# Performance work log

Measured on AMD Instinct MI355X. Metric: run time of the kernel, lower is better.

Reference implementation:

```python
import jax, jax.numpy as jnp
import numpy as np

N, D_MODEL, D_HIDDEN = 2048, 4096, 32768

def setup_inputs() -> dict:
    key = jax.random.key(0)
    k1, k2, k3, k4 = jax.random.split(key, 4)
    x = jax.random.normal(k1, (N, D_MODEL), dtype=jnp.float32)
    W_enc = jax.random.normal(k2, (D_MODEL, D_HIDDEN), dtype=jnp.float32) * 0.02
    b_enc = jax.random.normal(k3, (D_HIDDEN,), dtype=jnp.float32) * 0.02
    b_dec = jax.random.normal(k4, (D_MODEL,), dtype=jnp.float32) * 0.02
    return {"x": x, "W_enc": W_enc, "b_enc": b_enc, "b_dec": b_dec, "k": 64}

def reference(x, W_enc, b_enc, b_dec, k):
    # pre-activation: (x - b_dec) @ W_enc + b_enc   -> [N, d_hidden]
    pre_act = (x - b_dec) @ W_enc + b_enc
    acts = jax.nn.relu(pre_act)
    vals, idx = jax.lax.top_k(acts, k)          # [N, k] each
    rows = jnp.arange(acts.shape[0])[:, None]    # [N, 1]
    sparse_features = jnp.zeros_like(pre_act).at[rows, idx].set(vals)
    return sparse_features
```

## Files before the change

kernel.cpp:

```cpp
#include <hip/hip_runtime.h>
#include <hip/hip_fp16.h>

#define DEV __device__ __forceinline__

typedef __attribute__((ext_vector_type(8))) _Float16 half8;
typedef __attribute__((ext_vector_type(4))) _Float16 half4;
typedef __attribute__((ext_vector_type(4))) float floatx4;

static constexpr int M = 2048;
static constexpr int N = 32768;
static constexpr int K = 4096;

DEV void async_copy16(void* lds, const void* g) {
  __builtin_amdgcn_global_load_lds(
      (const __attribute__((address_space(1))) unsigned int*)g,
      (__attribute__((address_space(3))) unsigned int*)lds, 16, 0, 0);
}

__global__ void prep_x(const float* __restrict__ x, const float* __restrict__ b_dec,
                       _Float16* __restrict__ A1, _Float16* __restrict__ A2) {
  int i = blockIdx.x * blockDim.x + threadIdx.x;
  int idx = i * 4;
  float4 xv = *(const float4*)(x + idx);
  float4 bd = *(const float4*)(b_dec + (idx & (K - 1)));
  float c[4] = {xv.x - bd.x, xv.y - bd.y, xv.z - bd.z, xv.w - bd.w};
  half4 a1, a2;
#pragma unroll
  for (int j = 0; j < 4; ++j) {
    float s = c[j] * 0.03125f;
    _Float16 h1 = (_Float16)s;
    a1[j] = h1;
    a2[j] = (_Float16)((s - (float)h1) * 4096.0f);
  }
  *(half4*)(A1 + idx) = a1;
  *(half4*)(A2 + idx) = a2;
}

__global__ void prep_w(const float* __restrict__ W, _Float16* __restrict__ W1T,
                       _Float16* __restrict__ W2T) {
  __shared__ float tile[64][68];
  int tid = threadIdx.x;
  int tn = blockIdx.x & 511, tk = blockIdx.x >> 9;
  int k0 = tk * 64, n0 = tn * 64;
#pragma unroll
  for (int p = 0; p < 4; ++p) {
    int row = p * 16 + (tid >> 4);
    int col = (tid & 15) * 4;
    float4 v = *(const float4*)(W + (size_t)(k0 + row) * N + n0 + col);
    tile[row][col] = v.x; tile[row][col + 1] = v.y;
    tile[row][col + 2] = v.z; tile[row][col + 3] = v.w;
  }
  __syncthreads();
  int nl = tid >> 2, kc = (tid & 3) * 16;
  half8 v1[2], v2[2];
#pragma unroll
  for (int j = 0; j < 16; ++j) {
    float w = tile[kc + j][nl] * 32.0f;
    _Float16 h1 = (_Float16)w;
    _Float16 h2 = (_Float16)((w - (float)h1) * 4096.0f);
    v1[j >> 3][j & 7] = h1;
    v2[j >> 3][j & 7] = h2;
  }
  size_t off = (size_t)(n0 + nl) * K + k0 + kc;
  *(half8*)(W1T + off) = v1[0];
  *(half8*)(W1T + off + 8) = v1[1];
  *(half8*)(W2T + off) = v2[0];
  *(half8*)(W2T + off + 8) = v2[1];
}

__global__ __launch_bounds__(256) void gemm1(
    const _Float16* __restrict__ A, const _Float16* __restrict__ B,
    const float* __restrict__ b_enc, float* __restrict__ out) {
  __shared__ __align__(16) _Float16 lA[128 * 64];
  __shared__ __align__(16) _Float16 lB[128 * 64];
  const int tid = threadIdx.x;
  const int lane = tid & 63, wave = tid >> 6;
  const int wm = wave & 1, wn = wave >> 1;
  const int m0 = (blockIdx.x & 15) * 128, n0 = (blockIdx.x >> 4) * 128;

  floatx4 acc[4][4];
#pragma unroll
  for (int a = 0; a < 4; ++a)
#pragma unroll
    for (int b = 0; b < 4; ++b) acc[a][b] = (floatx4){0.f, 0.f, 0.f, 0.f};

  const int srow = lane >> 3;
  const int spos = lane & 7;
  const int quad = lane >> 4, l16 = lane & 15;

  for (int kk = 0; kk < K; kk += 64) {
#pragma unroll
    for (int i = 0; i < 4; ++i) {
      int ci = wave * 4 + i;
      int r = ci * 8 + srow;
      int ca = spos ^ srow;
      async_copy16(&lA[ci * 512], A + (size_t)(m0 + r) * K + kk + ca * 8);
      async_copy16(&lB[ci * 512], B + (size_t)(n0 + r) * K + kk + ca * 8);
    }
    __syncthreads();
#pragma unroll
    for (int s = 0; s < 2; ++s) {
      half8 af[4], bf[4];
#pragma unroll
      for (int f = 0; f < 4; ++f) {
        int row = wm * 64 + f * 16 + l16;
        int ch = ((s << 2) + quad) ^ (row & 7);
        af[f] = *(const half8*)&lA[row * 64 + ch * 8];
      }
#pragma unroll
      for (int f = 0; f < 4; ++f) {
        int row = wn * 64 + f * 16 + l16;
        int ch = ((s << 2) + quad) ^ (row & 7);
        bf[f] = *(const half8*)&lB[row * 64 + ch * 8];
      }
#pragma unroll
      for (int fm = 0; fm < 4; ++fm)
#pragma unroll
        for (int fn = 0; fn < 4; ++fn)
          acc[fm][fn] = __builtin_amdgcn_mfma_f32_16x16x32_f16(
              af[fm], bf[fn], acc[fm][fn], 0, 0, 0);
    }
    __syncthreads();
  }
  float bv[4];
#pragma unroll
  for (int fn = 0; fn < 4; ++fn) bv[fn] = b_enc[n0 + wn * 64 + fn * 16 + l16];
#pragma unroll
  for (int fm = 0; fm < 4; ++fm) {
    int rbase = m0 + wm * 64 + fm * 16 + quad * 4;
#pragma unroll
    for (int i = 0; i < 4; ++i) {
      float* orow = out + (size_t)(rbase + i) * N + n0 + wn * 64 + l16;
#pragma unroll
      for (int fn = 0; fn < 4; ++fn) orow[fn * 16] = acc[fm][fn][i] + bv[fn];
    }
  }
}

__global__ __launch_bounds__(256) void select_refine(
    const _Float16* __restrict__ A1, const _Float16* __restrict__ A2,
    const _Float16* __restrict__ W1T, const _Float16* __restrict__ W2T,
    const float* __restrict__ b_enc, float* __restrict__ out) {
  __shared__ int hist[4096];
  __shared__ __align__(16) _Float16 a1r[4096];
  __shared__ __align__(16) _Float16 a2r[4096];
  __shared__ float cval[256];
  __shared__ int cidx[256];
  __shared__ int gsum[256];
  __shared__ int Tbin, cnt;

  const int tid = threadIdx.x;
  const int row = blockIdx.x;
  float* rp = out + (size_t)row * N;

  const half8* a1g = (const half8*)(A1 + (size_t)row * K);
  const half8* a2g = (const half8*)(A2 + (size_t)row * K);
  for (int j = tid; j < K / 8; j += 256) {
    ((half8*)a1r)[j] = a1g[j];
    ((half8*)a2r)[j] = a2g[j];
  }
  for (int j = tid; j < 4096; j += 256) hist[j] = 0;
  if (tid == 0) { Tbin = 1; cnt = 0; }
  __syncthreads();

  for (int j = tid; j < N; j += 256) {
    float v = rp[j];
    if (v > 0.f) atomicAdd(&hist[__float_as_uint(v) >> 19], 1);
  }
  __syncthreads();
  int own = 0;
#pragma unroll
  for (int j = 0; j < 16; ++j) own += hist[tid * 16 + j];
  gsum[tid] = own;
  __syncthreads();
  for (int off = 1; off < 256; off <<= 1) {
    int add = (tid + off < 256) ? gsum[tid + off] : 0;
    __syncthreads();
    gsum[tid] += add;
    __syncthreads();
  }
  int acc = gsum[tid] - own;
  for (int j = 15; j >= 0; --j) {
    int h = hist[tid * 16 + j];
    acc += h;
    if (acc >= 64 && acc - h < 64) Tbin = tid * 16 + j;
  }
  __syncthreads();
  float thr = __uint_as_float((unsigned)Tbin << 19) - 0.01f;
  for (int j = tid; j < N; j += 256) {
    float v = rp[j];
    if (v > 0.f && v >= thr) {
      int p = atomicAdd(&cnt, 1);
      if (p < 256) cidx[p] = j;
    }
  }
  __syncthreads();
  const int nc = cnt < 256 ? cnt : 256;

  const int wave = tid >> 6, lane = tid & 63;
  for (int c = wave; c < nc; c += 4) {
    const int col = cidx[c];
    const half8* w1 = (const half8*)(W1T + (size_t)col * K);
    const half8* w2 = (const half8*)(W2T + (size_t)col * K);
    float a = 0.f;
#pragma unroll
    for (int j = 0; j < 8; ++j) {
      int off = j * 64 + lane;
      half8 hw1 = w1[off], hw2 = w2[off];
      half8 ha1 = ((const half8*)a1r)[off], ha2 = ((const half8*)a2r)[off];
#pragma unroll
      for (int e = 0; e < 8; ++e) {
        float sx = fmaf((float)ha2[e], 2.44140625e-4f, (float)ha1[e]);
        float tw = fmaf((float)hw2[e], 2.44140625e-4f, (float)hw1[e]);
        a = fmaf(sx, tw, a);
      }
    }
#pragma unroll
    for (int off = 32; off >= 1; off >>= 1) a += __shfl_xor(a, off);
    if (lane == 0) cval[c] = a + b_enc[col];
  }
  __syncthreads();

  float4 z = {0.f, 0.f, 0.f, 0.f};
  float4* rp4 = (float4*)rp;
  for (int j = tid; j < N / 4; j += 256) rp4[j] = z;
  __syncthreads();
  if (tid < nc) {
    float vi = cval[tid];
    int ii = cidx[tid];
    int rank = 0;
    for (int j = 0; j < nc; ++j) {
      float vj = cval[j];
      rank += (vj > vi) || (vj == vi && cidx[j] < ii);
    }
    if (rank < 64) rp[ii] = vi;
  }
}

extern "C" void kernel_launch(void* const* d_in, const int* in_sizes, int n_in,
                              void* d_out, int out_size, void* d_ws, size_t ws_size,
                              hipStream_t stream) {
  const float* x = (const float*)d_in[0];
  const float* W = (const float*)d_in[1];
  const float* b_enc = (const float*)d_in[2];
  const float* b_dec = (const float*)d_in[3];
  float* out = (float*)d_out;

  _Float16* A1 = (_Float16*)d_ws;
  _Float16* A2 = A1 + (size_t)M * K;
  _Float16* W1T = A2 + (size_t)M * K;
  _Float16* W2T = W1T + (size_t)N * K;

  prep_x<<<(M * K / 4) / 256, 256, 0, stream>>>(x, b_dec, A1, A2);
  prep_w<<<(N / 64) * (K / 64), 256, 0, stream>>>(W, W1T, W2T);
  gemm1<<<(M / 128) * (N / 128), 256, 0, stream>>>(A1, W1T, b_enc, out);
  select_refine<<<M, 256, 0, stream>>>(A1, A2, W1T, W2T, b_enc, out);
}
```

Before: 2.289 ms.

## Rewrite fp16 GEMM with 256x256 tiles, double-buffered async LDS pipeline

Result: faster. 2.205 ms (-3.7%).

```diff
diff --git a/kernel.cpp b/kernel.cpp
--- a/kernel.cpp
+++ b/kernel.cpp
@@ -68,66 +68,157 @@
   *(half8*)(W2T + off + 8) = v2[1];
 }
 
-__global__ __launch_bounds__(256) void gemm1(
+__global__ __launch_bounds__(512, 2) void gemm1(
     const _Float16* __restrict__ A, const _Float16* __restrict__ B,
     const float* __restrict__ b_enc, float* __restrict__ out) {
-  __shared__ __align__(16) _Float16 lA[128 * 64];
-  __shared__ __align__(16) _Float16 lB[128 * 64];
+  __shared__ __align__(16) _Float16 sA[2][256 * 32];
+  __shared__ __align__(16) _Float16 sB[2][256 * 32];
+
   const int tid = threadIdx.x;
   const int lane = tid & 63, wave = tid >> 6;
-  const int wm = wave & 1, wn = wave >> 1;
-  const int m0 = (blockIdx.x & 15) * 128, n0 = (blockIdx.x >> 4) * 128;
-
-  floatx4 acc[4][4];
-#pragma unroll
-  for (int a = 0; a < 4; ++a)
+  const int wm = wave >> 2, wn = wave & 3;
+  const int l16 = lane & 15, quad = lane >> 4;
+
+  const int swz = (blockIdx.x & 7) * 128 + (blockIdx.x >> 3);
+  const int m0 = (swz & 7) * 256, n0 = (swz >> 3) * 256;
+
+  floatx4 acc[8][4];
+#pragma unroll
+  for (int a = 0; a < 8; ++a)
 #pragma unroll
     for (int b = 0; b < 4; ++b) acc[a][b] = (floatx4){0.f, 0.f, 0.f, 0.f};
 
-  const int srow = lane >> 3;
-  const int spos = lane & 7;
-  const int quad = lane >> 4, l16 = lane & 15;
-
-  for (int kk = 0; kk < K; kk += 64) {
-#pragma unroll
-    for (int i = 0; i < 4; ++i) {
-      int ci = wave * 4 + i;
-      int r = ci * 8 + srow;
-      int ca = spos ^ srow;
-      async_copy16(&lA[ci * 512], A + (size_t)(m0 + r) * K + kk + ca * 8);
-      async_copy16(&lB[ci * 512], B + (size_t)(n0 + r) * K + kk + ca * 8);
-    }
-    __syncthreads();
-#pragma unroll
-    for (int s = 0; s < 2; ++s) {
-      half8 af[4], bf[4];
-#pragma unroll
-      for (int f = 0; f < 4; ++f) {
-        int row = wm * 64 + f * 16 + l16;
-        int ch = ((s << 2) + quad) ^ (row & 7);
-        af[f] = *(const half8*)&lA[row * 64 + ch * 8];
-      }
-#pragma unroll
-      for (int f = 0; f < 4; ++f) {
-        int row = wn * 64 + f * 16 + l16;
-        int ch = ((s << 2) + quad) ^ (row & 7);
-        bf[f] = *(const half8*)&lB[row * 64 + ch * 8];
-      }
-#pragma unroll
-      for (int fm = 0; fm < 4; ++fm)
-#pragma unroll
-        for (int fn = 0; fn < 4; ++fn)
-          acc[fm][fn] = __builtin_amdgcn_mfma_f32_16x16x32_f16(
-              af[fm], bf[fn], acc[fm][fn], 0, 0, 0);
-    }
-    __syncthreads();
-  }
+  const int srow = lane >> 2;
+  const int schunk = (lane & 3) ^ ((lane >> 3) & 3);
+  const int rg0 = (wave * 2 + 0) * 16 + srow;
+  const int rg1 = (wave * 2 + 1) * 16 + srow;
+  const _Float16* gA0 = A + (size_t)(m0 + rg0) * K + schunk * 8;
+  const _Float16* gA1 = A + (size_t)(m0 + rg1) * K + schunk * 8;
+  const _Float16* gB0 = B + (size_t)(n0 + rg0) * K + schunk * 8;
+  const _Float16* gB1 = B + (size_t)(n0 + rg1) * K + schunk * 8;
+  const int dG0 = (wave * 2 + 0) * 16 * 32;
+  const int dG1 = (wave * 2 + 1) * 16 * 32;
+
+  const int rslot = (quad ^ ((l16 >> 1) & 3)) * 8;
+  const int aoff = (wm * 128 + l16) * 32 + rslot;
+  const int boff = (wn * 64 + l16) * 32 + rslot;
+
+  async_copy16(&sA[0][dG0], gA0);
+  async_copy16(&sA[0][dG1], gA1);
+  async_copy16(&sB[0][dG0], gB0);
+  async_copy16(&sB[0][dG1], gB1);
+  async_copy16(&sB[1][dG0], gB0 + 32);
+  async_copy16(&sB[1][dG1], gB1 + 32);
+  asm volatile("s_waitcnt vmcnt(2)" ::: "memory");
+  __builtin_amdgcn_s_barrier();
+
+  constexpr int NS = K / 32;
+  half8 af[4], bf[4];
+
+  for (int s = 0; s < NS - 2; ++s) {
+    const int cur = s & 1;
+#pragma unroll
+    for (int f = 0; f < 4; ++f)
+      af[f] = *(const half8*)(sA[cur] + aoff + f * 512);
+#pragma unroll
+    for (int f = 0; f < 4; ++f)
+      bf[f] = *(const half8*)(sB[cur] + boff + f * 512);
+    async_copy16(&sA[cur ^ 1][dG0], gA0 + (s + 1) * 32);
+    async_copy16(&sA[cur ^ 1][dG1], gA1 + (s + 1) * 32);
+    __builtin_amdgcn_s_setprio(1);
+#pragma unroll
+    for (int fm = 0; fm < 4; ++fm)
+#pragma unroll
+      for (int fn = 0; fn < 4; ++fn)
+        acc[fm][fn] = __builtin_amdgcn_mfma_f32_16x16x32_f16(
+            af[fm], bf[fn], acc[fm][fn], 0, 0, 0);
+    __builtin_amdgcn_s_setprio(0);
+    asm volatile("s_waitcnt lgkmcnt(0)" ::: "memory");
+    __builtin_amdgcn_s_barrier();
+#pragma unroll
+    for (int f = 0; f < 4; ++f)
+      af[f] = *(const half8*)(sA[cur] + aoff + 2048 + f * 512);
+    async_copy16(&sB[cur][dG0], gB0 + (s + 2) * 32);
+    async_copy16(&sB[cur][dG1], gB1 + (s + 2) * 32);
+    __builtin_amdgcn_s_setprio(1);
+#pragma unroll
+    for (int fm = 0; fm < 4; ++fm)
+#pragma unroll
+      for (int fn = 0; fn < 4; ++fn)
+        acc[4 + fm][fn] = __builtin_amdgcn_mfma_f32_16x16x32_f16(
+            af[fm], bf[fn], acc[4 + fm][fn], 0, 0, 0);
+    __builtin_amdgcn_s_setprio(0);
+    asm volatile("s_waitcnt vmcnt(2) lgkmcnt(0)" ::: "memory");
+    __builtin_amdgcn_s_barrier();
+  }
+
+  {
+    const int cur = (NS - 2) & 1;
+#pragma unroll
+    for (int f = 0; f < 4; ++f)
+      af[f] = *(const half8*)(sA[cur] + aoff + f * 512);
+#pragma unroll
+    for (int f = 0; f < 4; ++f)
+      bf[f] = *(const half8*)(sB[cur] + boff + f * 512);
+    async_copy16(&sA[cur ^ 1][dG0], gA0 + (NS - 1) * 32);
+    async_copy16(&sA[cur ^ 1][dG1], gA1 + (NS - 1) * 32);
+    __builtin_amdgcn_s_setprio(1);
+#pragma unroll
+    for (int fm = 0; fm < 4; ++fm)
+#pragma unroll
+      for (int fn = 0; fn < 4; ++fn)
+        acc[fm][fn] = __builtin_amdgcn_mfma_f32_16x16x32_f16(
+            af[fm], bf[fn], acc[fm][fn], 0, 0, 0);
+    __builtin_amdgcn_s_setprio(0);
+    asm volatile("s_waitcnt lgkmcnt(0)" ::: "memory");
+    __builtin_amdgcn_s_barrier();
+#pragma unroll
+    for (int f = 0; f < 4; ++f)
+      af[f] = *(const half8*)(sA[cur] + aoff + 2048 + f * 512);
+    __builtin_amdgcn_s_setprio(1);
+#pragma unroll
+    for (int fm = 0; fm < 4; ++fm)
+#pragma unroll
+      for (int fn = 0; fn < 4; ++fn)
+        acc[4 + fm][fn] = __builtin_amdgcn_mfma_f32_16x16x32_f16(
+            af[fm], bf[fn], acc[4 + fm][fn], 0, 0, 0);
+    __builtin_amdgcn_s_setprio(0);
+    asm volatile("s_waitcnt vmcnt(0) lgkmcnt(0)" ::: "memory");
+    __builtin_amdgcn_s_barrier();
+  }
+  {
+    const int cur = (NS - 1) & 1;
+#pragma unroll
+    for (int f = 0; f < 4; ++f)
+      af[f] = *(const half8*)(sA[cur] + aoff + f * 512);
+#pragma unroll
+    for (int f = 0; f < 4; ++f)
+      bf[f] = *(const half8*)(sB[cur] + boff + f * 512);
+    __builtin_amdgcn_s_setprio(1);
+#pragma unroll
+    for (int fm = 0; fm < 4; ++fm)
+#pragma unroll
+      for (int fn = 0; fn < 4; ++fn)
+        acc[fm][fn] = __builtin_amdgcn_mfma_f32_16x16x32_f16(
+            af[fm], bf[fn], acc[fm][fn], 0, 0, 0);
+#pragma unroll
+    for (int f = 0; f < 4; ++f)
+      af[f] = *(const half8*)(sA[cur] + aoff + 2048 + f * 512);
+#pragma unroll
+    for (int fm = 0; fm < 4; ++fm)
+#pragma unroll
+      for (int fn = 0; fn < 4; ++fn)
+        acc[4 + fm][fn] = __builtin_amdgcn_mfma_f32_16x16x32_f16(
+            af[fm], bf[fn], acc[4 + fm][fn], 0, 0, 0);
+    __builtin_amdgcn_s_setprio(0);
+  }
+
   float bv[4];
 #pragma unroll
   for (int fn = 0; fn < 4; ++fn) bv[fn] = b_enc[n0 + wn * 64 + fn * 16 + l16];
 #pragma unroll
-  for (int fm = 0; fm < 4; ++fm) {
-    int rbase = m0 + wm * 64 + fm * 16 + quad * 4;
+  for (int fm = 0; fm < 8; ++fm) {
+    const int rbase = m0 + wm * 128 + fm * 16 + quad * 4;
 #pragma unroll
     for (int i = 0; i < 4; ++i) {
       float* orow = out + (size_t)(rbase + i) * N + n0 + wn * 64 + l16;
@@ -253,6 +344,6 @@
 
   prep_x<<<(M * K / 4) / 256, 256, 0, stream>>>(x, b_dec, A1, A2);
   prep_w<<<(N / 64) * (K / 64), 256, 0, stream>>>(W, W1T, W2T);
-  gemm1<<<(M / 128) * (N / 128), 256, 0, stream>>>(A1, W1T, b_enc, out);
+  gemm1<<<(M / 256) * (N / 256), 512, 0, stream>>>(A1, W1T, b_enc, out);
   select_refine<<<M, 256, 0, stream>>>(A1, A2, W1T, W2T, b_enc, out);
 }
```

## Rewrite gemm1 as 256x256-tile, 4-stage async-LDS pipelined kernel with 8 waves

Applied to the files above, without the earlier changes.

Measured after the change: 2.047 ms. 1.12x faster.

```diff
diff --git a/kernel.cpp b/kernel.cpp
--- a/kernel.cpp
+++ b/kernel.cpp
@@ -16,6 +16,12 @@
       (const __attribute__((address_space(1))) unsigned int*)g,
       (__attribute__((address_space(3))) unsigned int*)lds, 16, 0, 0);
 }
+
+#define BAR() __builtin_amdgcn_s_barrier()
+#define LGKM0() asm volatile("s_waitcnt lgkmcnt(0)" ::: "memory")
+#define VMW(n) asm volatile("s_waitcnt vmcnt(" #n ")" ::: "memory")
+#define PRIO1() __builtin_amdgcn_s_setprio(1)
+#define PRIO0() __builtin_amdgcn_s_setprio(0)
 
 __global__ void prep_x(const float* __restrict__ x, const float* __restrict__ b_dec,
                        _Float16* __restrict__ A1, _Float16* __restrict__ A2) {
@@ -68,66 +74,127 @@
   *(half8*)(W2T + off + 8) = v2[1];
 }
 
-__global__ __launch_bounds__(256) void gemm1(
+__global__ __launch_bounds__(512, 2) void gemm1(
     const _Float16* __restrict__ A, const _Float16* __restrict__ B,
     const float* __restrict__ b_enc, float* __restrict__ out) {
-  __shared__ __align__(16) _Float16 lA[128 * 64];
-  __shared__ __align__(16) _Float16 lB[128 * 64];
+  __shared__ __align__(16) _Float16 sA[4][8192];
+  __shared__ __align__(16) _Float16 sB[4][8192];
+
   const int tid = threadIdx.x;
   const int lane = tid & 63, wave = tid >> 6;
-  const int wm = wave & 1, wn = wave >> 1;
-  const int m0 = (blockIdx.x & 15) * 128, n0 = (blockIdx.x >> 4) * 128;
-
-  floatx4 acc[4][4];
-#pragma unroll
-  for (int a = 0; a < 4; ++a)
+  const int wm = wave >> 2, wn = wave & 3;
+  const int l16 = lane & 15, quad = lane >> 4;
+
+  const int swz = (blockIdx.x & 7) * 128 + (blockIdx.x >> 3);
+  const int m0 = (swz & 7) * 256, n0 = (swz >> 3) * 256;
+
+  floatx4 acc[8][4];
+#pragma unroll
+  for (int a = 0; a < 8; ++a)
 #pragma unroll
     for (int b = 0; b < 4; ++b) acc[a][b] = (floatx4){0.f, 0.f, 0.f, 0.f};
 
-  const int srow = lane >> 3;
-  const int spos = lane & 7;
-  const int quad = lane >> 4, l16 = lane & 15;
-
-  for (int kk = 0; kk < K; kk += 64) {
-#pragma unroll
-    for (int i = 0; i < 4; ++i) {
-      int ci = wave * 4 + i;
-      int r = ci * 8 + srow;
-      int ca = spos ^ srow;
-      async_copy16(&lA[ci * 512], A + (size_t)(m0 + r) * K + kk + ca * 8);
-      async_copy16(&lB[ci * 512], B + (size_t)(n0 + r) * K + kk + ca * 8);
-    }
-    __syncthreads();
-#pragma unroll
-    for (int s = 0; s < 2; ++s) {
-      half8 af[4], bf[4];
-#pragma unroll
-      for (int f = 0; f < 4; ++f) {
-        int row = wm * 64 + f * 16 + l16;
-        int ch = ((s << 2) + quad) ^ (row & 7);
-        af[f] = *(const half8*)&lA[row * 64 + ch * 8];
-      }
-#pragma unroll
-      for (int f = 0; f < 4; ++f) {
-        int row = wn * 64 + f * 16 + l16;
-        int ch = ((s << 2) + quad) ^ (row & 7);
-        bf[f] = *(const half8*)&lB[row * 64 + ch * 8];
-      }
-#pragma unroll
-      for (int fm = 0; fm < 4; ++fm)
-#pragma unroll
-        for (int fn = 0; fn < 4; ++fn)
-          acc[fm][fn] = __builtin_amdgcn_mfma_f32_16x16x32_f16(
-              af[fm], bf[fn], acc[fm][fn], 0, 0, 0);
-    }
-    __syncthreads();
-  }
+  const int srow = lane >> 2;
+  const int schunk = (lane & 3) ^ ((lane >> 3) & 3);
+  const _Float16* pA = A + (size_t)(m0 + wave * 16 + srow) * K + schunk * 8;
+  const _Float16* pB = B + (size_t)(n0 + wave * 16 + srow) * K + schunk * 8;
+  const _Float16* pA2 = pA + (size_t)128 * K;
+  const _Float16* pB2 = pB + (size_t)128 * K;
+
+  const int rslot = (quad ^ ((l16 >> 1) & 3)) * 8;
+  const int aBase = (wm * 128 + l16) * 32 + rslot;
+  const int bBase = (wn * 64 + l16) * 32 + rslot;
+
+  half8 af[4], bf[4];
+
+  auto stageA = [&](int bk, int koff) {
+    async_copy16(&sA[bk][wave * 512], pA + koff);
+    async_copy16(&sA[bk][4096 + wave * 512], pA2 + koff);
+  };
+  auto stageB = [&](int bk, int koff) {
+    async_copy16(&sB[bk][wave * 512], pB + koff);
+    async_copy16(&sB[bk][4096 + wave * 512], pB2 + koff);
+  };
+  auto readA = [&](int bk, int qm) {
+#pragma unroll
+    for (int f = 0; f < 4; ++f)
+      af[f] = *(const half8*)&sA[bk][aBase + qm * 2048 + f * 512];
+  };
+  auto readB = [&](int bk) {
+#pragma unroll
+    for (int f = 0; f < 4; ++f)
+      bf[f] = *(const half8*)&sB[bk][bBase + f * 512];
+  };
+  auto mfma4 = [&](int r0) {
+#pragma unroll
+    for (int fm = 0; fm < 4; ++fm)
+#pragma unroll
+      for (int fn = 0; fn < 4; ++fn)
+        acc[r0 + fm][fn] = __builtin_amdgcn_mfma_f32_16x16x32_f16(
+            af[fm], bf[fn], acc[r0 + fm][fn], 0, 0, 0);
+  };
+
+  stageA(0, 0);  stageB(0, 0);
+  stageA(1, 32); stageB(1, 32);
+  stageA(2, 64); stageB(2, 64);
+  VMW(8);
+  BAR();
+
+  for (int i = 0; i < 31; ++i) {
+    const int kA = i * 128;
+    readA(0, 0); readB(0);
+    stageA(3, kA + 96);
+    BAR(); LGKM0(); PRIO1(); mfma4(0); PRIO0(); BAR();
+    readA(0, 1);
+    stageB(3, kA + 96);
+    BAR(); LGKM0(); PRIO1(); mfma4(4); PRIO0(); VMW(8); BAR();
+    readA(1, 0); readB(1);
+    stageA(0, kA + 128);
+    BAR(); LGKM0(); PRIO1(); mfma4(0); PRIO0(); BAR();
+    readA(1, 1);
+    stageB(0, kA + 128);
+    BAR(); LGKM0(); PRIO1(); mfma4(4); PRIO0(); VMW(8); BAR();
+    readA(2, 0); readB(2);
+    stageA(1, kA + 160);
+    BAR(); LGKM0(); PRIO1(); mfma4(0); PRIO0(); BAR();
+    readA(2, 1);
+    stageB(1, kA + 160);
+    BAR(); LGKM0(); PRIO1(); mfma4(4); PRIO0(); VMW(8); BAR();
+    readA(3, 0); readB(3);
+    stageA(2, kA + 192);
+    BAR(); LGKM0(); PRIO1(); mfma4(0); PRIO0(); BAR();
+    readA(3, 1);
+    stageB(2, kA + 192);
+    BAR(); LGKM0(); PRIO1(); mfma4(4); PRIO0(); VMW(8); BAR();
+  }
+
+  {
+    readA(0, 0); readB(0);
+    stageA(3, 4064);
+    BAR(); LGKM0(); PRIO1(); mfma4(0); PRIO0(); BAR();
+    readA(0, 1);
+    stageB(3, 4064);
+    BAR(); LGKM0(); PRIO1(); mfma4(4); PRIO0(); VMW(8); BAR();
+    readA(1, 0); readB(1);
+    BAR(); LGKM0(); PRIO1(); mfma4(0); PRIO0(); BAR();
+    readA(1, 1);
+    BAR(); LGKM0(); PRIO1(); mfma4(4); PRIO0(); VMW(4); BAR();
+    readA(2, 0); readB(2);
+    BAR(); LGKM0(); PRIO1(); mfma4(0); PRIO0(); BAR();
+    readA(2, 1);
+    BAR(); LGKM0(); PRIO1(); mfma4(4); PRIO0(); VMW(0); BAR();
+    readA(3, 0); readB(3);
+    BAR(); LGKM0(); PRIO1(); mfma4(0); PRIO0(); BAR();
+    readA(3, 1);
+    LGKM0(); PRIO1(); mfma4(4); PRIO0();
+  }
+
   float bv[4];
 #pragma unroll
   for (int fn = 0; fn < 4; ++fn) bv[fn] = b_enc[n0 + wn * 64 + fn * 16 + l16];
 #pragma unroll
-  for (int fm = 0; fm < 4; ++fm) {
-    int rbase = m0 + wm * 64 + fm * 16 + quad * 4;
+  for (int fm = 0; fm < 8; ++fm) {
+    const int rbase = m0 + wm * 128 + fm * 16 + quad * 4;
 #pragma unroll
     for (int i = 0; i < 4; ++i) {
       float* orow = out + (size_t)(rbase + i) * N + n0 + wn * 64 + l16;
@@ -253,6 +320,6 @@
 
   prep_x<<<(M * K / 4) / 256, 256, 0, stream>>>(x, b_dec, A1, A2);
   prep_w<<<(N / 64) * (K / 64), 256, 0, stream>>>(W, W1T, W2T);
-  gemm1<<<(M / 128) * (N / 128), 256, 0, stream>>>(A1, W1T, b_enc, out);
+  gemm1<<<(M / 256) * (N / 256), 512, 0, stream>>>(A1, W1T, b_enc, out);
   select_refine<<<M, 256, 0, stream>>>(A1, A2, W1T, W2T, b_enc, out);
 }
```
